# Optimization experiments

Measured on AMD Instinct MI355X. Metric: run time of the kernel, lower is better.

The kernel has to match this reference:

```python
import jax, jax.numpy as jnp
import numpy as np

DIM = 768
HEADS = 12
HEAD_DIM = DIM // HEADS
SCALE = HEAD_DIM ** -0.5


def setup_inputs() -> dict:
    key = jax.random.key(0)
    ks = jax.random.split(key, 6)
    B, N, M, C = 4, 2048, 1024, DIM
    x = jax.random.normal(ks[0], (B, N, C), dtype=jnp.float32)
    r = jax.random.normal(ks[1], (B, M, C), dtype=jnp.float32)
    s = 1.0 / np.sqrt(C)
    W_q = jax.random.normal(ks[2], (C, C), dtype=jnp.float32) * s
    W_kv = jax.random.normal(ks[3], (C, 2 * C), dtype=jnp.float32) * s
    W_proj = jax.random.normal(ks[4], (C, C), dtype=jnp.float32) * s
    b_proj = jax.random.normal(ks[5], (C,), dtype=jnp.float32) * 0.02
    return {"x": x, "r": r, "W_q": W_q, "W_kv": W_kv, "W_proj": W_proj, "b_proj": b_proj}


def reference(x, r, W_q, W_kv, W_proj, b_proj):
    B, N, C = x.shape
    _, M, _ = r.shape
    H, D = HEADS, C // HEADS
    # projections (no bias on q/kv per qkv_bias=False)
    q = (x @ W_q).reshape(B, N, H, D)            # bnhd
    kv = (r @ W_kv).reshape(B, M, 2, H, D)
    k = kv[:, :, 0]                               # bmhd
    v = kv[:, :, 1]                               # bmhd
    attn = jnp.einsum('bnhd,bmhd->bhnm', q, k) * SCALE
    attn = jax.nn.softmax(attn, axis=-1)
    out = jnp.einsum('bhnm,bmhd->bnhd', attn, v).reshape(B, N, C)
    return out @ W_proj + b_proj
```

## Files before the change

### kernel.cpp

```cpp
#include <hip/hip_runtime.h>
#include <hip/hip_bf16.h>
#include <cstdint>

#define HEADS 12

typedef __attribute__((ext_vector_type(8))) __bf16 bf16x8;
typedef __attribute__((ext_vector_type(4))) __bf16 bf16x4;
typedef __attribute__((ext_vector_type(4))) float f32x4;
typedef __attribute__((ext_vector_type(16))) float f32x16;

#define AS1 __attribute__((address_space(1)))
#define AS3 __attribute__((address_space(3)))

__device__ __forceinline__ void gload16(const void* src, void* lds) {
  __builtin_amdgcn_global_load_lds((AS1 void*)src, (AS3 void*)lds, 16, 0, 0);
}

__device__ __forceinline__ uint32_t cvtpk(float lo, float hi) {
  uint32_t r;
  asm("v_cvt_pk_bf16_f32 %0, %1, %2" : "=v"(r) : "v"(lo), "v"(hi));
  return r;
}

__device__ __forceinline__ float exp2_fast(float x) {
  float r;
  asm("v_exp_f32 %0, %1" : "=v"(r) : "v"(x));
  return r;
}

__global__ void k_cast2(const float* __restrict__ x, const float* __restrict__ r,
                        __bf16* __restrict__ xb, __bf16* __restrict__ rb) {
  int i = (blockIdx.x * 256 + threadIdx.x) * 4;
  const float* src;
  __bf16* dst;
  int off;
  if (i < 6291456) { src = x; dst = xb; off = i; }
  else             { src = r; dst = rb; off = i - 6291456; }
  float4 v = *(const float4*)(src + off);
  bf16x4 o;
  o[0] = (__bf16)v.x; o[1] = (__bf16)v.y; o[2] = (__bf16)v.z; o[3] = (__bf16)v.w;
  *(bf16x4*)(dst + off) = o;
}

__global__ void k_twc3(const float* __restrict__ Wq, const float* __restrict__ Wkv,
                       const float* __restrict__ Wp, __bf16* __restrict__ wqt,
                       __bf16* __restrict__ wkvt, __bf16* __restrict__ wpt) {
  __shared__ float tile[32][33];
  const float* W; __bf16* Wt; int N; float scale;
  if (blockIdx.z == 0)      { W = Wq;  Wt = wqt;  N = 768;  scale = 0.18033688011112042f; }
  else if (blockIdx.z == 1) { W = Wkv; Wt = wkvt; N = 1536; scale = 1.0f; }
  else                      { W = Wp;  Wt = wpt;  N = 768;  scale = 1.0f; }
  int nt = blockIdx.x, kt = blockIdx.y;
  if (nt * 32 >= N) return;
  int c = threadIdx.x & 31, r0 = threadIdx.x >> 5;
#pragma unroll
  for (int i = 0; i < 4; ++i) {
    int r = r0 + i * 8;
    tile[r][c] = W[(size_t)(kt * 32 + r) * N + nt * 32 + c];
  }
  __syncthreads();
#pragma unroll
  for (int i = 0; i < 4; ++i) {
    int r = r0 + i * 8;
    Wt[(size_t)(nt * 32 + r) * 768 + kt * 32 + c] = (__bf16)(tile[c][r] * scale);
  }
}

__global__ __launch_bounds__(256, 2) void k_gemm12(
    const __bf16* __restrict__ xb, const __bf16* __restrict__ rb,
    const __bf16* __restrict__ wqt, const __bf16* __restrict__ wkvt,
    __bf16* __restrict__ qb, __bf16* __restrict__ kvb, __bf16* __restrict__ vTp) {
  __shared__ __align__(16) char ldsA[2][16384];
  __shared__ __align__(16) char ldsB[2][16384];
  const int tid = threadIdx.x;
  const int ln = tid & 63;
  const int w = tid >> 6;
  int id = blockIdx.x;
  id = (id & 7) * 96 + (id >> 3);
  const __bf16* A; const __bf16* Bt; __bf16* C; int N, bm0, bn0; bool qpart;
  if (id < 384) { A = xb; Bt = wqt;  C = qb;  N = 768;  bm0 = (id / 6) * 128;  bn0 = (id % 6) * 128;  qpart = true; }
  else { int i2 = id - 384; A = rb; Bt = wkvt; C = kvb; N = 1536; bm0 = (i2 / 12) * 128; bn0 = (i2 % 12) * 128; qpart = false; }
  const int wm0 = (w >> 1) * 64, wn0 = (w & 1) * 64;

  auto stage = [&](char* lds, const __bf16* G, int row0, int k0) {
    const char* gb = (const char*)(G + (size_t)row0 * 768 + k0);
#pragma unroll
    for (int c = 0; c < 4; ++c) {
      int off = c * 4096 + tid * 16;
      int row = off >> 7;
      int s = ((off >> 4) & 7) ^ (row & 7);
      gload16(gb + (size_t)row * 1536 + (s << 4), lds + c * 4096 + (w << 10));
    }
  };

  f32x4 acc[4][4] = {};
  stage(ldsA[0], A, bm0, 0);
  stage(ldsB[0], Bt, bn0, 0);
  __syncthreads();
  for (int kt = 0; kt < 12; ++kt) {
    const char* bufA = ldsA[kt & 1];
    const char* bufB = ldsB[kt & 1];
    if (kt + 1 < 12) {
      stage(ldsA[(kt + 1) & 1], A, bm0, (kt + 1) << 6);
      stage(ldsB[(kt + 1) & 1], Bt, bn0, (kt + 1) << 6);
    }
    bf16x8 af[2][4], bf[2][4];
#pragma unroll
    for (int kk = 0; kk < 2; ++kk)
#pragma unroll
      for (int mt = 0; mt < 4; ++mt) {
        int row = wm0 + mt * 16 + (ln & 15);
        af[kk][mt] = *(const bf16x8*)(bufA + row * 128 + (((kk * 4 + (ln >> 4)) ^ (row & 7)) << 4));
      }
#pragma unroll
    for (int kk = 0; kk < 2; ++kk)
#pragma unroll
      for (int nt = 0; nt < 4; ++nt) {
        int row = wn0 + nt * 16 + (ln & 15);
        bf[kk][nt] = *(const bf16x8*)(bufB + row * 128 + (((kk * 4 + (ln >> 4)) ^ (row & 7)) << 4));
      }
    __builtin_amdgcn_s_setprio(1);
#pragma unroll
    for (int kk = 0; kk < 2; ++kk)
#pragma unroll
      for (int mt = 0; mt < 4; ++mt)
#pragma unroll
        for (int nt = 0; nt < 4; ++nt)
          acc[mt][nt] = __builtin_amdgcn_mfma_f32_16x16x32_bf16(af[kk][mt], bf[kk][nt], acc[mt][nt], 0, 0, 0);
    __builtin_amdgcn_s_setprio(0);
    __syncthreads();
  }
#pragma unroll
  for (int mt = 0; mt < 4; ++mt) {
    int row = bm0 + wm0 + mt * 16 + ((ln >> 4) << 2);
#pragma unroll
    for (int nt = 0; nt < 4; ++nt) {
      int col = bn0 + wn0 + nt * 16 + (ln & 15);
      if (!qpart && bn0 >= 768) {
        bf16x4 o;
#pragma unroll
        for (int jj = 0; jj < 4; ++jj) o[jj] = (__bf16)acc[mt][nt][jj];
        *(bf16x4*)(vTp + ((size_t)((row >> 10) * 768 + col - 768)) * 1024 + (row & 1023)) = o;
      } else {
#pragma unroll
        for (int jj = 0; jj < 4; ++jj)
          C[(size_t)(row + jj) * N + col] = (__bf16)acc[mt][nt][jj];
      }
    }
  }
}

__global__ __launch_bounds__(256, 2) void k_gemmP(
    const __bf16* __restrict__ A, const __bf16* __restrict__ Bt,
    float* __restrict__ C, const float* __restrict__ bias) {
  __shared__ __align__(16) char ldsA[2][16384];
  __shared__ __align__(16) char ldsB[2][16384];
  const int tid = threadIdx.x;
  const int ln = tid & 63;
  const int w = tid >> 6;
  int bid = blockIdx.y * 6 + blockIdx.x;
  bid = (bid & 7) * 48 + (bid >> 3);
  const int bm0 = (bid / 6) * 128, bn0 = (bid % 6) * 128;
  const int wm0 = (w >> 1) * 64, wn0 = (w & 1) * 64;

  auto stage = [&](char* lds, const __bf16* G, int row0, int k0) {
    const char* gb = (const char*)(G + (size_t)row0 * 768 + k0);
#pragma unroll
    for (int c = 0; c < 4; ++c) {
      int off = c * 4096 + tid * 16;
      int row = off >> 7;
      int s = ((off >> 4) & 7) ^ (row & 7);
      gload16(gb + (size_t)row * 1536 + (s << 4), lds + c * 4096 + (w << 10));
    }
  };

  f32x4 acc[4][4] = {};
  stage(ldsA[0], A, bm0, 0);
  stage(ldsB[0], Bt, bn0, 0);
  __syncthreads();
  for (int kt = 0; kt < 12; ++kt) {
    const char* bufA = ldsA[kt & 1];
    const char* bufB = ldsB[kt & 1];
    if (kt + 1 < 12) {
      stage(ldsA[(kt + 1) & 1], A, bm0, (kt + 1) << 6);
      stage(ldsB[(kt + 1) & 1], Bt, bn0, (kt + 1) << 6);
    }
    bf16x8 af[2][4], bf[2][4];
#pragma unroll
    for (int kk = 0; kk < 2; ++kk)
#pragma unroll
      for (int mt = 0; mt < 4; ++mt) {
        int row = wm0 + mt * 16 + (ln & 15);
        af[kk][mt] = *(const bf16x8*)(bufA + row * 128 + (((kk * 4 + (ln >> 4)) ^ (row & 7)) << 4));
      }
#pragma unroll
    for (int kk = 0; kk < 2; ++kk)
#pragma unroll
      for (int nt = 0; nt < 4; ++nt) {
        int row = wn0 + nt * 16 + (ln & 15);
        bf[kk][nt] = *(const bf16x8*)(bufB + row * 128 + (((kk * 4 + (ln >> 4)) ^ (row & 7)) << 4));
      }
    __builtin_amdgcn_s_setprio(1);
#pragma unroll
    for (int kk = 0; kk < 2; ++kk)
#pragma unroll
      for (int mt = 0; mt < 4; ++mt)
#pragma unroll
        for (int nt = 0; nt < 4; ++nt)
          acc[mt][nt] = __builtin_amdgcn_mfma_f32_16x16x32_bf16(af[kk][mt], bf[kk][nt], acc[mt][nt], 0, 0, 0);
    __builtin_amdgcn_s_setprio(0);
    __syncthreads();
  }
#pragma unroll
  for (int mt = 0; mt < 4; ++mt) {
    int row = bm0 + wm0 + mt * 16 + ((ln >> 4) << 2);
#pragma unroll
    for (int nt = 0; nt < 4; ++nt) {
      int col = bn0 + wn0 + nt * 16 + (ln & 15);
      float bv = bias[col];
#pragma unroll
      for (int jj = 0; jj < 4; ++jj)
        C[(size_t)(row + jj) * 768 + col] = acc[mt][nt][jj] + bv;
    }
  }
}

__global__ __launch_bounds__(256, 4) void k_attn(
    const __bf16* __restrict__ q, const __bf16* __restrict__ kv,
    const __bf16* __restrict__ vT, __bf16* __restrict__ ao) {
  __shared__ __align__(16) char ldsK[3][4096];
  __shared__ __align__(16) char ldsV[3][4096];
  const int tid = threadIdx.x, ln = tid & 63, w = tid >> 6;
  const int l5 = ln >> 5, l32 = ln & 31;
  int id = blockIdx.y * 16 + blockIdx.x;
  id = (id & 7) * 96 + (id >> 3);
  const int qt = id & 15, bh = id >> 4;
  const int b = bh / HEADS, h = bh % HEADS;
  const int qrow = b * 2048 + qt * 128 + w * 32 + l32;

  const char* kgb = (const char*)(kv + ((size_t)b * 1024) * 1536 + h * 64);
  const char* vgb = (const char*)(vT + ((size_t)(b * 768 + h * 64)) * 1024);

  const int krow = tid >> 3, kc = tid & 7;
  const size_t ksrc = (size_t)krow * 3072 + (size_t)(((kc ^ (krow & 7)) << 4));
  const int vrow = tid >> 2, vc = tid & 3;
  const size_t vsrc = (size_t)vrow * 2048 + (size_t)(((vc ^ ((vrow >> 1) & 3)) << 4));
  const int ldst = w << 10;

  auto stageKV = [&](int t, int buf) {
    gload16(kgb + (size_t)t * 98304 + ksrc, ldsK[buf] + ldst);
    gload16(vgb + (size_t)t * 64 + vsrc, ldsV[buf] + ldst);
  };

  bf16x8 qf[4];
#pragma unroll
  for (int s = 0; s < 4; ++s)
    qf[s] = *(const bf16x8*)(q + (size_t)qrow * 768 + h * 64 + 16 * s + 8 * l5);

  stageKV(0, 0);
  stageKV(1, 1);

  f32x16 accO[2] = {};
  float mrow = -1e30f, lrow = 0.f;

  asm volatile("s_waitcnt vmcnt(2)" ::: "memory");
  __builtin_amdgcn_s_barrier();

  for (int t = 0; t < 32; ++t) {
    if (t < 30) stageKV(t + 2, (t + 2) % 3);
    const char* bufK = ldsK[t % 3];
    const char* bufV = ldsV[t % 3];

    f32x16 s16 = {};
    __builtin_amdgcn_s_setprio(1);
#pragma unroll
    for (int s = 0; s < 4; ++s) {
      bf16x8 kf = *(const bf16x8*)(bufK + l32 * 128 + (((2 * s + l5) ^ (l32 & 7)) << 4));
      s16 = __builtin_amdgcn_mfma_f32_32x32x16_bf16(kf, qf[s], s16, 0, 0, 0);
    }
    __builtin_amdgcn_s_setprio(0);

    float lm = s16[0];
#pragma unroll
    for (int i = 1; i < 16; ++i) lm = fmaxf(lm, s16[i]);
    if (!__all(lm <= mrow + 8.0f)) {
      float mx = fmaxf(lm, __shfl_xor(lm, 32, 64));
      float mn = fmaxf(mrow, mx);
      float corr = exp2_fast(mrow - mn);
      mrow = mn;
      lrow *= corr;
#pragma unroll
      for (int dt = 0; dt < 2; ++dt)
#pragma unroll
        for (int i = 0; i < 16; ++i) accO[dt][i] *= corr;
    }
    float p[16];
    float ps = 0.f;
#pragma unroll
    for (int i = 0; i < 16; ++i) {
      p[i] = exp2_fast(s16[i] - mrow);
      ps += p[i];
    }
    lrow += ps;

    uint32_t c0[4], c1[4];
#pragma unroll
    for (int j = 0; j < 4; ++j) {
      c0[j] = cvtpk(p[4 * j], p[4 * j + 1]);
      c1[j] = cvtpk(p[4 * j + 2], p[4 * j + 3]);
    }
    uint32_t w00 = c0[0], w02 = c0[1];
    asm("v_permlane32_swap_b32 %0, %1" : "+v"(w00), "+v"(w02));
    uint32_t w01 = c1[0], w03 = c1[1];
    asm("v_permlane32_swap_b32 %0, %1" : "+v"(w01), "+v"(w03));
    uint32_t w10 = c0[2], w12 = c0[3];
    asm("v_permlane32_swap_b32 %0, %1" : "+v"(w10), "+v"(w12));
    uint32_t w11 = c1[2], w13 = c1[3];
    asm("v_permlane32_swap_b32 %0, %1" : "+v"(w11), "+v"(w13));
    union { uint32_t u[4]; bf16x8 v; } pk0, pk1;
    pk0.u[0] = w00; pk0.u[1] = w01; pk0.u[2] = w02; pk0.u[3] = w03;
    pk1.u[0] = w10; pk1.u[1] = w11; pk1.u[2] = w12; pk1.u[3] = w13;

    __builtin_amdgcn_s_setprio(1);
#pragma unroll
    for (int dt = 0; dt < 2; ++dt) {
      int vr = dt * 32 + l32;
      bf16x8 vf0 = *(const bf16x8*)(bufV + vr * 64 + (((0 + l5) ^ ((vr >> 1) & 3)) << 4));
      accO[dt] = __builtin_amdgcn_mfma_f32_32x32x16_bf16(vf0, pk0.v, accO[dt], 0, 0, 0);
      bf16x8 vf1 = *(const bf16x8*)(bufV + vr * 64 + (((2 + l5) ^ ((vr >> 1) & 3)) << 4));
      accO[dt] = __builtin_amdgcn_mfma_f32_32x32x16_bf16(vf1, pk1.v, accO[dt], 0, 0, 0);
    }
    __builtin_amdgcn_s_setprio(0);

    if (t < 30) {
      asm volatile("s_waitcnt vmcnt(2)" ::: "memory");
      __builtin_amdgcn_s_barrier();
    } else if (t == 30) {
      asm volatile("s_waitcnt vmcnt(0)" ::: "memory");
      __builtin_amdgcn_s_barrier();
    }
  }

  float l = lrow + __shfl_xor(lrow, 32, 64);
  float inv = 1.0f / l;
  size_t rowb = (size_t)qrow * 768 + h * 64;
#pragma unroll
  for (int dt = 0; dt < 2; ++dt)
#pragma unroll
    for (int j = 0; j < 4; ++j) {
      bf16x4 o;
#pragma unroll
      for (int i = 0; i < 4; ++i) o[i] = (__bf16)(accO[dt][4 * j + i] * inv);
      *(bf16x4*)(ao + rowb + dt * 32 + 8 * j + 4 * l5) = o;
    }
}

extern "C" void kernel_launch(void* const* d_in, const int* in_sizes, int n_in,
                              void* d_out, int out_size, void* d_ws, size_t ws_size,
                              hipStream_t stream) {
  const float* x = (const float*)d_in[0];
  const float* r = (const float*)d_in[1];
  const float* Wq = (const float*)d_in[2];
  const float* Wkv = (const float*)d_in[3];
  const float* Wp = (const float*)d_in[4];
  const float* bp = (const float*)d_in[5];

  char* ws = (char*)d_ws;
  __bf16* xb  = (__bf16*)ws; ws += (size_t)6291456 * 2;
  __bf16* rb  = (__bf16*)ws; ws += (size_t)3145728 * 2;
  __bf16* wqt = (__bf16*)ws; ws += (size_t)589824 * 2;
  __bf16* wkvt= (__bf16*)ws; ws += (size_t)1179648 * 2;
  __bf16* wpt = (__bf16*)ws; ws += (size_t)589824 * 2;
  __bf16* qb  = (__bf16*)ws; ws += (size_t)6291456 * 2;
  __bf16* kvb = (__bf16*)ws; ws += (size_t)6291456 * 2;
  __bf16* vT  = (__bf16*)ws; ws += (size_t)3145728 * 2;
  __bf16* ao  = (__bf16*)ws;

  k_cast2<<<9216, 256, 0, stream>>>(x, r, xb, rb);
  k_twc3<<<dim3(48, 24, 3), 256, 0, stream>>>(Wq, Wkv, Wp, wqt, wkvt, wpt);
  k_gemm12<<<768, 256, 0, stream>>>(xb, rb, wqt, wkvt, qb, kvb, vT);
  k_attn<<<dim3(16, 48), 256, 0, stream>>>(qb, kvb, vT, ao);
  k_gemmP<<<dim3(6, 64), 256, 0, stream>>>(ao, wpt, (float*)d_out, bp);
}
```

Before: 102.4 us.

## Write K/V in MFMA-fragment tiled layout and process 64-key tiles in attention

The QKV GEMM epilogue now writes K and V into per-(batch,head) tiles already arranged in the MFMA operand fragment order, so attention can stage K with contiguous unswizzled loads and read V fragments straight from global memory into registers. The attention loop handles 64 keys per iteration (two score tiles), which halves the number of barriers and iterations, and it drops V from LDS. In exchange it raises register pressure (occupancy hint lowered from 4 to 3 blocks), leaves V global loads exposed on the critical path, and makes the GEMM epilogue stores more scattered.

Result: no change. 101.0 us (-1.3%).

```diff
diff --git a/kernel.cpp b/kernel.cpp
--- a/kernel.cpp
+++ b/kernel.cpp
@@ -69,7 +69,7 @@
 __global__ __launch_bounds__(256, 2) void k_gemm12(
     const __bf16* __restrict__ xb, const __bf16* __restrict__ rb,
     const __bf16* __restrict__ wqt, const __bf16* __restrict__ wkvt,
-    __bf16* __restrict__ qb, __bf16* __restrict__ kvb, __bf16* __restrict__ vTp) {
+    __bf16* __restrict__ qb, __bf16* __restrict__ kbp, __bf16* __restrict__ vbp) {
   __shared__ __align__(16) char ldsA[2][16384];
   __shared__ __align__(16) char ldsB[2][16384];
   const int tid = threadIdx.x;
@@ -77,9 +77,9 @@
   const int w = tid >> 6;
   int id = blockIdx.x;
   id = (id & 7) * 96 + (id >> 3);
-  const __bf16* A; const __bf16* Bt; __bf16* C; int N, bm0, bn0; bool qpart;
-  if (id < 384) { A = xb; Bt = wqt;  C = qb;  N = 768;  bm0 = (id / 6) * 128;  bn0 = (id % 6) * 128;  qpart = true; }
-  else { int i2 = id - 384; A = rb; Bt = wkvt; C = kvb; N = 1536; bm0 = (i2 / 12) * 128; bn0 = (i2 % 12) * 128; qpart = false; }
+  const __bf16* A; const __bf16* Bt; int bm0, bn0; bool qpart;
+  if (id < 384) { A = xb; Bt = wqt;  bm0 = (id / 6) * 128;  bn0 = (id % 6) * 128;  qpart = true; }
+  else { int i2 = id - 384; A = rb; Bt = wkvt; bm0 = (i2 / 12) * 128; bn0 = (i2 % 12) * 128; qpart = false; }
   const int wm0 = (w >> 1) * 64, wn0 = (w & 1) * 64;
 
   auto stage = [&](char* lds, const __bf16* G, int row0, int k0) {
@@ -136,15 +136,30 @@
 #pragma unroll
     for (int nt = 0; nt < 4; ++nt) {
       int col = bn0 + wn0 + nt * 16 + (ln & 15);
-      if (!qpart && bn0 >= 768) {
-        bf16x4 o;
-#pragma unroll
-        for (int jj = 0; jj < 4; ++jj) o[jj] = (__bf16)acc[mt][nt][jj];
-        *(bf16x4*)(vTp + ((size_t)((row >> 10) * 768 + col - 768)) * 1024 + (row & 1023)) = o;
+      if (qpart) {
+#pragma unroll
+        for (int jj = 0; jj < 4; ++jj)
+          qb[(size_t)(row + jj) * 768 + col] = (__bf16)acc[mt][nt][jj];
       } else {
-#pragma unroll
-        for (int jj = 0; jj < 4; ++jj)
-          C[(size_t)(row + jj) * N + col] = (__bf16)acc[mt][nt][jj];
+        int bb = row >> 10, kvg = row & 1023;
+        int t32 = kvg >> 5, kvl = kvg & 31;
+        if (col < 768) {
+          int hh = col >> 6, d = col & 63;
+          size_t base = ((size_t)(bb * 12 + hh) * 32 + t32) * 2048
+                      + (size_t)(((((d >> 4) << 1) + ((d >> 3) & 1)) * 32 + kvl) * 8 + (d & 7));
+#pragma unroll
+          for (int jj = 0; jj < 4; ++jj)
+            kbp[base + jj * 8] = (__bf16)acc[mt][nt][jj];
+        } else {
+          int cv = col - 768;
+          int hh = cv >> 6, d = cv & 63;
+          size_t base = ((size_t)(bb * 12 + hh) * 32 + t32) * 2048
+                      + (size_t)((((((d >> 5) << 1) + (kvl >> 4)) * 2 + ((kvl >> 3) & 1)) * 32 + (d & 31)) * 8 + (kvl & 7));
+          bf16x4 o;
+#pragma unroll
+          for (int jj = 0; jj < 4; ++jj) o[jj] = (__bf16)acc[mt][nt][jj];
+          *(bf16x4*)(vbp + base) = o;
+        }
       }
     }
   }
@@ -225,31 +240,25 @@
   }
 }
 
-__global__ __launch_bounds__(256, 4) void k_attn(
-    const __bf16* __restrict__ q, const __bf16* __restrict__ kv,
-    const __bf16* __restrict__ vT, __bf16* __restrict__ ao) {
-  __shared__ __align__(16) char ldsK[3][4096];
-  __shared__ __align__(16) char ldsV[3][4096];
-  const int tid = threadIdx.x, ln = tid & 63, w = tid >> 6;
-  const int l5 = ln >> 5, l32 = ln & 31;
+__global__ __launch_bounds__(256, 3) void k_attn(
+    const __bf16* __restrict__ q, const __bf16* __restrict__ kb,
+    const __bf16* __restrict__ vb, __bf16* __restrict__ ao) {
+  __shared__ __align__(16) char ldsK[3][8192];
+  const int tid = threadIdx.x, ln = tid & 63;
+  const int l5 = ln >> 5, l32 = ln & 31, w = tid >> 6;
   int id = blockIdx.y * 16 + blockIdx.x;
   id = (id & 7) * 96 + (id >> 3);
   const int qt = id & 15, bh = id >> 4;
   const int b = bh / HEADS, h = bh % HEADS;
   const int qrow = b * 2048 + qt * 128 + w * 32 + l32;
 
-  const char* kgb = (const char*)(kv + ((size_t)b * 1024) * 1536 + h * 64);
-  const char* vgb = (const char*)(vT + ((size_t)(b * 768 + h * 64)) * 1024);
-
-  const int krow = tid >> 3, kc = tid & 7;
-  const size_t ksrc = (size_t)krow * 3072 + (size_t)(((kc ^ (krow & 7)) << 4));
-  const int vrow = tid >> 2, vc = tid & 3;
-  const size_t vsrc = (size_t)vrow * 2048 + (size_t)(((vc ^ ((vrow >> 1) & 3)) << 4));
-  const int ldst = w << 10;
-
-  auto stageKV = [&](int t, int buf) {
-    gload16(kgb + (size_t)t * 98304 + ksrc, ldsK[buf] + ldst);
-    gload16(vgb + (size_t)t * 64 + vsrc, ldsV[buf] + ldst);
+  const char* kbase = (const char*)kb + (size_t)bh * 131072;
+  const __bf16* vbase = vb + (size_t)bh * 65536;
+  const int vchunk = l5 * 256 + l32 * 8;
+
+  auto stageK = [&](int t, int buf) {
+    gload16(kbase + (size_t)t * 8192 + tid * 16, ldsK[buf] + tid * 16);
+    gload16(kbase + (size_t)t * 8192 + 4096 + tid * 16, ldsK[buf] + 4096 + tid * 16);
   };
 
   bf16x8 qf[4];
@@ -257,32 +266,47 @@
   for (int s = 0; s < 4; ++s)
     qf[s] = *(const bf16x8*)(q + (size_t)qrow * 768 + h * 64 + 16 * s + 8 * l5);
 
-  stageKV(0, 0);
-  stageKV(1, 1);
+  stageK(0, 0);
+  stageK(1, 1);
 
   f32x16 accO[2] = {};
   float mrow = -1e30f, lrow = 0.f;
 
-  asm volatile("s_waitcnt vmcnt(2)" ::: "memory");
+  asm volatile("s_waitcnt vmcnt(0)" ::: "memory");
   __builtin_amdgcn_s_barrier();
 
-  for (int t = 0; t < 32; ++t) {
-    if (t < 30) stageKV(t + 2, (t + 2) % 3);
+  for (int t = 0; t < 16; ++t) {
     const char* bufK = ldsK[t % 3];
-    const char* bufV = ldsV[t % 3];
-
-    f32x16 s16 = {};
+
+    bf16x8 vf[2][2][2];
+    {
+      const __bf16* vt = vbase + (size_t)(2 * t) * 2048 + vchunk;
+#pragma unroll
+      for (int nt = 0; nt < 2; ++nt)
+#pragma unroll
+        for (int dt = 0; dt < 2; ++dt)
+#pragma unroll
+          for (int ks = 0; ks < 2; ++ks)
+            vf[nt][dt][ks] = *(const bf16x8*)(vt + nt * 2048 + (dt * 2 + ks) * 512);
+    }
+    if (t < 14) stageK(t + 2, (t + 2) % 3);
+
+    f32x16 s16[2] = {};
     __builtin_amdgcn_s_setprio(1);
 #pragma unroll
     for (int s = 0; s < 4; ++s) {
-      bf16x8 kf = *(const bf16x8*)(bufK + l32 * 128 + (((2 * s + l5) ^ (l32 & 7)) << 4));
-      s16 = __builtin_amdgcn_mfma_f32_32x32x16_bf16(kf, qf[s], s16, 0, 0, 0);
+      bf16x8 kf0 = *(const bf16x8*)(bufK + (s * 2 + l5) * 512 + l32 * 16);
+      s16[0] = __builtin_amdgcn_mfma_f32_32x32x16_bf16(kf0, qf[s], s16[0], 0, 0, 0);
+      bf16x8 kf1 = *(const bf16x8*)(bufK + 4096 + (s * 2 + l5) * 512 + l32 * 16);
+      s16[1] = __builtin_amdgcn_mfma_f32_32x32x16_bf16(kf1, qf[s], s16[1], 0, 0, 0);
     }
     __builtin_amdgcn_s_setprio(0);
 
-    float lm = s16[0];
-#pragma unroll
-    for (int i = 1; i < 16; ++i) lm = fmaxf(lm, s16[i]);
+    float lm = s16[0][0];
+#pragma unroll
+    for (int nt = 0; nt < 2; ++nt)
+#pragma unroll
+      for (int i = 0; i < 16; ++i) lm = fmaxf(lm, s16[nt][i]);
     if (!__all(lm <= mrow + 8.0f)) {
       float mx = fmaxf(lm, __shfl_xor(lm, 32, 64));
       float mn = fmaxf(mrow, mx);
@@ -294,51 +318,53 @@
 #pragma unroll
         for (int i = 0; i < 16; ++i) accO[dt][i] *= corr;
     }
-    float p[16];
     float ps = 0.f;
 #pragma unroll
-    for (int i = 0; i < 16; ++i) {
-      p[i] = exp2_fast(s16[i] - mrow);
-      ps += p[i];
-    }
+    for (int nt = 0; nt < 2; ++nt)
+#pragma unroll
+      for (int i = 0; i < 16; ++i) {
+        float e = exp2_fast(s16[nt][i] - mrow);
+        s16[nt][i] = e;
+        ps += e;
+      }
     lrow += ps;
 
-    uint32_t c0[4], c1[4];
-#pragma unroll
-    for (int j = 0; j < 4; ++j) {
-      c0[j] = cvtpk(p[4 * j], p[4 * j + 1]);
-      c1[j] = cvtpk(p[4 * j + 2], p[4 * j + 3]);
-    }
-    uint32_t w00 = c0[0], w02 = c0[1];
-    asm("v_permlane32_swap_b32 %0, %1" : "+v"(w00), "+v"(w02));
-    uint32_t w01 = c1[0], w03 = c1[1];
-    asm("v_permlane32_swap_b32 %0, %1" : "+v"(w01), "+v"(w03));
-    uint32_t w10 = c0[2], w12 = c0[3];
-    asm("v_permlane32_swap_b32 %0, %1" : "+v"(w10), "+v"(w12));
-    uint32_t w11 = c1[2], w13 = c1[3];
-    asm("v_permlane32_swap_b32 %0, %1" : "+v"(w11), "+v"(w13));
-    union { uint32_t u[4]; bf16x8 v; } pk0, pk1;
-    pk0.u[0] = w00; pk0.u[1] = w01; pk0.u[2] = w02; pk0.u[3] = w03;
-    pk1.u[0] = w10; pk1.u[1] = w11; pk1.u[2] = w12; pk1.u[3] = w13;
+    bf16x8 pk[2][2];
+#pragma unroll
+    for (int nt = 0; nt < 2; ++nt) {
+      uint32_t c0[4], c1[4];
+#pragma unroll
+      for (int j = 0; j < 4; ++j) {
+        c0[j] = cvtpk(s16[nt][4 * j], s16[nt][4 * j + 1]);
+        c1[j] = cvtpk(s16[nt][4 * j + 2], s16[nt][4 * j + 3]);
+      }
+      uint32_t w00 = c0[0], w02 = c0[1];
+      asm("v_permlane32_swap_b32 %0, %1" : "+v"(w00), "+v"(w02));
+      uint32_t w01 = c1[0], w03 = c1[1];
+      asm("v_permlane32_swap_b32 %0, %1" : "+v"(w01), "+v"(w03));
+      uint32_t w10 = c0[2], w12 = c0[3];
+      asm("v_permlane32_swap_b32 %0, %1" : "+v"(w10), "+v"(w12));
+      uint32_t w11 = c1[2], w13 = c1[3];
+      asm("v_permlane32_swap_b32 %0, %1" : "+v"(w11), "+v"(w13));
+      union { uint32_t u[4]; bf16x8 v; } pk0, pk1;
+      pk0.u[0] = w00; pk0.u[1] = w01; pk0.u[2] = w02; pk0.u[3] = w03;
+      pk1.u[0] = w10; pk1.u[1] = w11; pk1.u[2] = w12; pk1.u[3] = w13;
+      pk[nt][0] = pk0.v;
+      pk[nt][1] = pk1.v;
+    }
 
     __builtin_amdgcn_s_setprio(1);
 #pragma unroll
-    for (int dt = 0; dt < 2; ++dt) {
-      int vr = dt * 32 + l32;
-      bf16x8 vf0 = *(const bf16x8*)(bufV + vr * 64 + (((0 + l5) ^ ((vr >> 1) & 3)) << 4));
-      accO[dt] = __builtin_amdgcn_mfma_f32_32x32x16_bf16(vf0, pk0.v, accO[dt], 0, 0, 0);
-      bf16x8 vf1 = *(const bf16x8*)(bufV + vr * 64 + (((2 + l5) ^ ((vr >> 1) & 3)) << 4));
-      accO[dt] = __builtin_amdgcn_mfma_f32_32x32x16_bf16(vf1, pk1.v, accO[dt], 0, 0, 0);
-    }
+    for (int nt = 0; nt < 2; ++nt)
+#pragma unroll
+      for (int ks = 0; ks < 2; ++ks) {
+        accO[0] = __builtin_amdgcn_mfma_f32_32x32x16_bf16(vf[nt][0][ks], pk[nt][ks], accO[0], 0, 0, 0);
+        accO[1] = __builtin_amdgcn_mfma_f32_32x32x16_bf16(vf[nt][1][ks], pk[nt][ks], accO[1], 0, 0, 0);
+      }
     __builtin_amdgcn_s_setprio(0);
 
-    if (t < 30) {
-      asm volatile("s_waitcnt vmcnt(2)" ::: "memory");
-      __builtin_amdgcn_s_barrier();
-    } else if (t == 30) {
-      asm volatile("s_waitcnt vmcnt(0)" ::: "memory");
-      __builtin_amdgcn_s_barrier();
-    }
+    __builtin_amdgcn_sched_barrier(0);
+    __builtin_amdgcn_s_barrier();
   }
 
   float l = lrow + __shfl_xor(lrow, 32, 64);
@@ -372,13 +398,13 @@
   __bf16* wkvt= (__bf16*)ws; ws += (size_t)1179648 * 2;
   __bf16* wpt = (__bf16*)ws; ws += (size_t)589824 * 2;
   __bf16* qb  = (__bf16*)ws; ws += (size_t)6291456 * 2;
-  __bf16* kvb = (__bf16*)ws; ws += (size_t)6291456 * 2;
-  __bf16* vT  = (__bf16*)ws; ws += (size_t)3145728 * 2;
+  __bf16* kbk = (__bf16*)ws; ws += (size_t)3145728 * 2;
+  __bf16* vbk = (__bf16*)ws; ws += (size_t)3145728 * 2;
   __bf16* ao  = (__bf16*)ws;
 
   k_cast2<<<9216, 256, 0, stream>>>(x, r, xb, rb);
   k_twc3<<<dim3(48, 24, 3), 256, 0, stream>>>(Wq, Wkv, Wp, wqt, wkvt, wpt);
-  k_gemm12<<<768, 256, 0, stream>>>(xb, rb, wqt, wkvt, qb, kvb, vT);
-  k_attn<<<dim3(16, 48), 256, 0, stream>>>(qb, kvb, vT, ao);
+  k_gemm12<<<768, 256, 0, stream>>>(xb, rb, wqt, wkvt, qb, kbk, vbk);
+  k_attn<<<dim3(16, 48), 256, 0, stream>>>(qb, kbk, vbk, ao);
   k_gemmP<<<dim3(6, 64), 256, 0, stream>>>(ao, wpt, (float*)d_out, bp);
 }
```
